# Kernel optimization log

Hardware: AMD Instinct MI355X
Metric: run time of the kernel (lower is better)

Reference implementation:

```python
import jax, jax.numpy as jnp
import numpy as np

B, N, X_DIM, Y_DIM, K = 256, 65536, 32, 64, 8
SIGMA_INIT = 0.01

def setup_inputs() -> dict:
    key = jax.random.key(0)
    k1, k2, k3, k4 = jax.random.split(key, 4)
    return {
        "x": jax.random.normal(k1, (B, X_DIM), dtype=jnp.float32),
        "pos_matrix": jax.random.normal(k2, (N, X_DIM), dtype=jnp.float32),
        "project_matrix": jax.random.normal(k3, (N, X_DIM, K), dtype=jnp.float32),
        "color_matrix": jax.random.normal(k4, (N, Y_DIM), dtype=jnp.float32),
        "sigma_matrix": jnp.full((N, K), SIGMA_INIT, dtype=jnp.float32),
    }

def reference(x, pos_matrix, project_matrix, color_matrix, sigma_matrix):
    # x_diff = (x[:,None,:] - pos[None,:,:]) @ P  -> (B, N, k)
    # computed without materializing (B, N, x_dim):
    xP = jnp.einsum('bi,nio->bno', x, project_matrix)          # (B, N, k)
    posP = jnp.einsum('ni,nio->no', pos_matrix, project_matrix)  # (N, k)
    x_diff = xP - posP[None, :, :]                               # (B, N, k)
    # Gaussian kernel per modality
    g = jnp.exp(-x_diff ** 2 / (2.0 * sigma_matrix ** 2))        # (B, N, k)
    # color = g^T @ color_matrix per batch -> (B, k, y_dim)
    color = jnp.einsum('bnk,ny->bky', g, color_matrix)
    return color
```

## Files before the change

kernel.cpp:

```cpp
#include <hip/hip_runtime.h>


typedef __attribute__((ext_vector_type(8))) short short8;
typedef __attribute__((ext_vector_type(4))) float f32x4;

#define NTOT   65536
#define XD     32
#define YD     64
#define KK     8
#define META_BYTES (NTOT*KK*8)
#define PART_FLOATS 32768
#define NCHUNKS 2048
#define CSTR   40

__device__ __forceinline__ void gload16(const void* g, void* l) {
  __builtin_amdgcn_global_load_lds(
      (const __attribute__((address_space(1))) unsigned*)g,
      (__attribute__((address_space(3))) unsigned*)l, 16, 0, 0);
}

union FragU { unsigned u[4]; short8 s8; };

__global__ __launch_bounds__(256)
void gaf_pre(const float* __restrict__ pos, const float* __restrict__ proj,
             const float* __restrict__ sig, float2* __restrict__ meta) {
  int gid = blockIdx.x * 256 + threadIdx.x;
  int n = gid >> 3, k = gid & 7;
  const float*  pk = proj + (size_t)n * XD * KK + k;
  const float4* pg = (const float4*)(pos + (size_t)n * XD);
  float d = 0.f;
#pragma unroll
  for (int j = 0; j < 8; ++j) {
    float4 v = pg[j];
    d = fmaf(v.x, pk[(4*j+0)*KK], d);
    d = fmaf(v.y, pk[(4*j+1)*KK], d);
    d = fmaf(v.z, pk[(4*j+2)*KK], d);
    d = fmaf(v.w, pk[(4*j+3)*KK], d);
  }
  float s = sig[gid];
  meta[gid] = make_float2(d, -0.72134752044448169f / (s * s));
}

__global__ __launch_bounds__(512, 4)
void gaf_main(const float* __restrict__ x, const float* __restrict__ proj,
              const float* __restrict__ colr, const float2* __restrict__ meta,
              float* __restrict__ partial, int NCH, int NR) {
  __shared__ __align__(16) unsigned short sPool[16*512*2 + 64*CSTR];
  __shared__ float sPosP[8][36];
  __shared__ float sInv[8][36];
  __shared__ __align__(16) float rawP[32*260];
  unsigned short* sPb0 = sPool;
  unsigned short* sPb1 = sPool + 16*512;
  unsigned short (*sCol)[CSTR] = (unsigned short(*)[CSTR])(sPool + 2*16*512);

  const int t = threadIdx.x, l = t & 63, w = t >> 6;

  int nr, sblk;
  {
    const int gid = blockIdx.x;
    if ((NR & 7) == 0) {
      const int xcd = gid & 7, j = gid >> 3;
      nr   = xcd * (NR >> 3) + (j >> 2);
      sblk = j & 3;
    } else { nr = gid >> 2; sblk = gid & 3; }
  }

  const int bt = w & 3, k0 = (w >> 2) * 4;
  const int lc = l & 15, lg = l >> 4;
  const int cbeg = nr * NCH;
  int cend = cbeg + NCH; if (cend > NCHUNKS) cend = NCHUNKS;

  float* pb = partial + (size_t)(nr * 4 + sblk) * PART_FLOATS;
  if (cbeg >= cend) {
    float4 z = {0.f,0.f,0.f,0.f};
#pragma unroll
    for (int r = 0; r < PART_FLOATS/4/512; ++r) ((float4*)pb)[t + r*512] = z;
    return;
  }

  short8 xf0, xf1;
  {
    const int brow = sblk*64 + bt*16 + lc;
    const float4* xr = (const float4*)(x + (size_t)brow*XD + lg*8);
    float4 u0 = xr[0], u1 = xr[1];
    float xv[8] = {u0.x,u0.y,u0.z,u0.w,u1.x,u1.y,u1.z,u1.w};
#pragma unroll
    for (int j = 0; j < 8; ++j) {
      unsigned u = __float_as_uint(xv[j]);
      unsigned short h0 = (unsigned short)(u >> 16);
      float r1 = xv[j] - __uint_as_float(u & 0xFFFF0000u);
      unsigned ur = __float_as_uint(r1);
      ur += 0x7FFFu + ((ur >> 16) & 1u);
      xf0[j] = (short)h0;
      xf1[j] = (short)(unsigned short)(ur >> 16);
    }
  }

  f32x4 acc[4][4];
#pragma unroll
  for (int a = 0; a < 4; ++a)
#pragma unroll
    for (int b = 0; b < 4; ++b) acc[a][b] = (f32x4){0.f,0.f,0.f,0.f};

  const int kp  = l & 1;
  const int ipL = (l >> 1) & 3;
  const int nS  = ((l >> 3) & 7) | ((w & 3) << 3);
  const int sS  = nS >> 4;
  const int ldst= (nS & 15);

  auto ISSUE_P = [&](int c) {
    const float4* Pg = (const float4*)(proj + (size_t)c * 32 * XD * KK);
#pragma unroll
    for (int r2 = 0; r2 < 4; ++r2) {
      const int nd = w + r2*8;
      gload16(Pg + nd*64 + l, &rawP[nd*260]);
    }
  };

  ISSUE_P(cbeg);
  for (int c = cbeg; c < cend; ++c) {
    __syncthreads();
    const int yq = w*8 + (l>>3);
    const int nq = (l&7)*4;
    const float* cb = colr + (size_t)(c*32 + nq)*YD + yq;
    float c0 = cb[0], c1 = cb[YD], c2 = cb[2*YD], c3 = cb[3*YD];
    float2 mpf;
    if (t < 256) mpf = meta[(size_t)c * 256 + t];
    {
      const float4* raw4 = (const float4*)rawP;
#pragma unroll
      for (int r = 0; r < 2; ++r) {
        const int ip = ipL | (((w >> 2) & 1) << 2) | (r << 3);
        const int f0 = nS * 65 + ip * 4 + kp;
        float4 va = raw4[f0], vb = raw4[f0 + 2];
        const int l_dst = ldst | ((ip >> 2) << 4);
        const int wd = ip & 3;
        float ea[4] = {va.x, va.y, va.z, va.w};
        float eb[4] = {vb.x, vb.y, vb.z, vb.w};
#pragma unroll
        for (int jj = 0; jj < 4; ++jj) {
          const int ks = (kp*4 + jj)*2 + sS;
          unsigned hi, lo;
          asm("v_cvt_pk_bf16_f32 %0, %1, %2" : "=v"(hi) : "v"(ea[jj]), "v"(eb[jj]));
          float r0 = ea[jj] - __uint_as_float(hi << 16);
          float r1 = eb[jj] - __uint_as_float(hi & 0xFFFF0000u);
          asm("v_cvt_pk_bf16_f32 %0, %1, %2" : "=v"(lo) : "v"(r0), "v"(r1));
          ((unsigned*)sPb0)[ks*256 + l_dst*4 + wd] = hi;
          ((unsigned*)sPb1)[ks*256 + l_dst*4 + wd] = lo;
        }
      }
    }
    {
      unsigned w0, w1;
      asm("v_cvt_pk_bf16_f32 %0, %1, %2" : "=v"(w0) : "v"(c0), "v"(c1));
      asm("v_cvt_pk_bf16_f32 %0, %1, %2" : "=v"(w1) : "v"(c2), "v"(c3));
      *(uint2*)&sCol[yq][nq] = make_uint2(w0, w1);
    }
    if (t < 256) { sPosP[t&7][t>>3] = mpf.x; sInv[t&7][t>>3] = mpf.y; }
    __syncthreads();
    if (c + 1 < cend) ISSUE_P(c + 1);

    __builtin_amdgcn_s_setprio(1);
#pragma unroll
    for (int kk = 0; kk < 4; ++kk) {
      const int k = k0 + kk;
      FragU gb;
      {
        short8 p0 = *(const short8*)&sPb0[(k*2+0)*512 + l*8];
        short8 p1 = *(const short8*)&sPb1[(k*2+0)*512 + l*8];
        f32x4 S = (f32x4){0.f,0.f,0.f,0.f};
        S = __builtin_amdgcn_mfma_f32_16x16x32_bf16(p1, xf1, S, 0, 0, 0);
        S = __builtin_amdgcn_mfma_f32_16x16x32_bf16(p1, xf0, S, 0, 0, 0);
        S = __builtin_amdgcn_mfma_f32_16x16x32_bf16(p0, xf1, S, 0, 0, 0);
        S = __builtin_amdgcn_mfma_f32_16x16x32_bf16(p0, xf0, S, 0, 0, 0);
        float4 pp = *(const float4*)&sPosP[k][lg*4];
        float4 iv = *(const float4*)&sInv[k][lg*4];
        float d0 = S[0]-pp.x, d1 = S[1]-pp.y, d2 = S[2]-pp.z, d3 = S[3]-pp.w;
        float g0 = __builtin_amdgcn_exp2f(d0*d0*iv.x);
        float g1 = __builtin_amdgcn_exp2f(d1*d1*iv.y);
        float g2 = __builtin_amdgcn_exp2f(d2*d2*iv.z);
        float g3 = __builtin_amdgcn_exp2f(d3*d3*iv.w);
        asm("v_cvt_pk_bf16_f32 %0, %1, %2" : "=v"(gb.u[0]) : "v"(g0), "v"(g1));
        asm("v_cvt_pk_bf16_f32 %0, %1, %2" : "=v"(gb.u[1]) : "v"(g2), "v"(g3));
      }
      {
        short8 p0 = *(const short8*)&sPb0[(k*2+1)*512 + l*8];
        short8 p1 = *(const short8*)&sPb1[(k*2+1)*512 + l*8];
        f32x4 S = (f32x4){0.f,0.f,0.f,0.f};
        S = __builtin_amdgcn_mfma_f32_16x16x32_bf16(p1, xf1, S, 0, 0, 0);
        S = __builtin_amdgcn_mfma_f32_16x16x32_bf16(p1, xf0, S, 0, 0, 0);
        S = __builtin_amdgcn_mfma_f32_16x16x32_bf16(p0, xf1, S, 0, 0, 0);
        S = __builtin_amdgcn_mfma_f32_16x16x32_bf16(p0, xf0, S, 0, 0, 0);
        float4 pp = *(const float4*)&sPosP[k][16 + lg*4];
        float4 iv = *(const float4*)&sInv[k][16 + lg*4];
        float d0 = S[0]-pp.x, d1 = S[1]-pp.y, d2 = S[2]-pp.z, d3 = S[3]-pp.w;
        float g0 = __builtin_amdgcn_exp2f(d0*d0*iv.x);
        float g1 = __builtin_amdgcn_exp2f(d1*d1*iv.y);
        float g2 = __builtin_amdgcn_exp2f(d2*d2*iv.z);
        float g3 = __builtin_amdgcn_exp2f(d3*d3*iv.w);
        asm("v_cvt_pk_bf16_f32 %0, %1, %2" : "=v"(gb.u[2]) : "v"(g0), "v"(g1));
        asm("v_cvt_pk_bf16_f32 %0, %1, %2" : "=v"(gb.u[3]) : "v"(g2), "v"(g3));
      }
#pragma unroll
      for (int ys = 0; ys < 4; ++ys) {
        FragU af;
        *(uint2*)&af.u[0] = *(const uint2*)&sCol[ys*16 + lc][lg*4];
        *(uint2*)&af.u[2] = *(const uint2*)&sCol[ys*16 + lc][16 + lg*4];
        acc[kk][ys] = __builtin_amdgcn_mfma_f32_16x16x32_bf16(af.s8, gb.s8,
                                                              acc[kk][ys], 0, 0, 0);
      }
    }
    __builtin_amdgcn_s_setprio(0);
  }
  __syncthreads();

  float* epi = (float*)sPool + w * (64*17);
#pragma unroll
  for (int kk = 0; kk < 4; ++kk) {
    const int k = k0 + kk;
#pragma unroll
    for (int ys = 0; ys < 4; ++ys) {
#pragma unroll
      for (int r = 0; r < 4; ++r)
        epi[(ys*16 + lg*4 + r)*17 + lc] = acc[kk][ys][r];
    }
    __syncthreads();
#pragma unroll
    for (int it = 0; it < 4; ++it) {
      int bi = it*4 + lg, y0 = lc*4;
      float4 v = { epi[(y0+0)*17 + bi], epi[(y0+1)*17 + bi],
                   epi[(y0+2)*17 + bi], epi[(y0+3)*17 + bi] };
      *(float4*)&pb[(size_t)(bt*16 + bi)*512 + k*64 + y0] = v;
    }
    __syncthreads();
  }
}

__global__ __launch_bounds__(512)
void gaf_reduce(const float* __restrict__ partial, float* __restrict__ out, int NR) {
  const int b = blockIdx.x;
  const int s = b >> 6, bl = b & 63;
  const int t = threadIdx.x;
  float a0 = 0.f, a1 = 0.f, a2 = 0.f, a3 = 0.f;
  int nr = 0;
  for (; nr + 4 <= NR; nr += 4) {
    a0 += partial[(size_t)((nr+0)*4 + s)*PART_FLOATS + bl*512 + t];
    a1 += partial[(size_t)((nr+1)*4 + s)*PART_FLOATS + bl*512 + t];
    a2 += partial[(size_t)((nr+2)*4 + s)*PART_FLOATS + bl*512 + t];
    a3 += partial[(size_t)((nr+3)*4 + s)*PART_FLOATS + bl*512 + t];
  }
  for (; nr < NR; ++nr)
    a0 += partial[(size_t)(nr*4 + s)*PART_FLOATS + bl*512 + t];
  out[(size_t)b*512 + t] = (a0 + a1) + (a2 + a3);
}

extern "C" void kernel_launch(void* const* d_in, const int* in_sizes, int n_in,
                              void* d_out, int out_size, void* d_ws, size_t ws_size,
                              hipStream_t stream) {
  const float* x    = (const float*)d_in[0];
  const float* pos  = (const float*)d_in[1];
  const float* proj = (const float*)d_in[2];
  const float* colr = (const float*)d_in[3];
  const float* sig  = (const float*)d_in[4];
  float* out = (float*)d_out;

  float2* meta    = (float2*)d_ws;
  float*  partial = (float*)((char*)d_ws + META_BYTES);

  size_t avail = (ws_size > META_BYTES) ? ws_size - META_BYTES : 0;
  int NR = (int)(avail / (4ull * PART_FLOATS * 4ull));
  if (NR > 128) NR = 128;
  if (NR < 1)  NR = 1;
  if (NR >= 8) NR &= ~7;
  int NCH = (NCHUNKS + NR - 1) / NR;

  gaf_pre<<<(NTOT*KK)/256, 256, 0, stream>>>(pos, proj, sig, meta);
  gaf_main<<<4*NR, 512, 0, stream>>>(x, proj, colr, meta, partial, NCH, NR);
  gaf_reduce<<<256, 512, 0, stream>>>(partial, out, NR);
}
```

Baseline: 100.0 us.

## Fuse posP and inverse-sigma precompute into main kernel, drop pre-pass

Removes the separate gaf_pre kernel that computed pos·P projections and inverse sigma terms into a workspace buffer. The main kernel now loads each chunk's pos rows asynchronously into LDS next to the projection tile it already stages, and computes the dot products and inverse sigma in-loop. This saves one kernel launch and a second full read of the projection matrix, at the cost of extra LDS, extra per-chunk ALU work and an LDS-bank-conflicted dot product on the critical path between barriers.

Result: no change. 99.67 us, median of 2 (-0.4%).

```diff
diff --git a/kernel.cpp b/kernel.cpp
--- a/kernel.cpp
+++ b/kernel.cpp
@@ -8,7 +8,6 @@
 #define XD     32
 #define YD     64
 #define KK     8
-#define META_BYTES (NTOT*KK*8)
 #define PART_FLOATS 32768
 #define NCHUNKS 2048
 #define CSTR   40
@@ -21,34 +20,16 @@
 
 union FragU { unsigned u[4]; short8 s8; };
 
-__global__ __launch_bounds__(256)
-void gaf_pre(const float* __restrict__ pos, const float* __restrict__ proj,
-             const float* __restrict__ sig, float2* __restrict__ meta) {
-  int gid = blockIdx.x * 256 + threadIdx.x;
-  int n = gid >> 3, k = gid & 7;
-  const float*  pk = proj + (size_t)n * XD * KK + k;
-  const float4* pg = (const float4*)(pos + (size_t)n * XD);
-  float d = 0.f;
-#pragma unroll
-  for (int j = 0; j < 8; ++j) {
-    float4 v = pg[j];
-    d = fmaf(v.x, pk[(4*j+0)*KK], d);
-    d = fmaf(v.y, pk[(4*j+1)*KK], d);
-    d = fmaf(v.z, pk[(4*j+2)*KK], d);
-    d = fmaf(v.w, pk[(4*j+3)*KK], d);
-  }
-  float s = sig[gid];
-  meta[gid] = make_float2(d, -0.72134752044448169f / (s * s));
-}
-
 __global__ __launch_bounds__(512, 4)
-void gaf_main(const float* __restrict__ x, const float* __restrict__ proj,
-              const float* __restrict__ colr, const float2* __restrict__ meta,
+void gaf_main(const float* __restrict__ x, const float* __restrict__ pos,
+              const float* __restrict__ proj, const float* __restrict__ colr,
+              const float* __restrict__ sig,
               float* __restrict__ partial, int NCH, int NR) {
   __shared__ __align__(16) unsigned short sPool[16*512*2 + 64*CSTR];
   __shared__ float sPosP[8][36];
   __shared__ float sInv[8][36];
   __shared__ __align__(16) float rawP[32*260];
+  __shared__ __align__(16) float rawPos[32*32];
   unsigned short* sPb0 = sPool;
   unsigned short* sPb1 = sPool + 16*512;
   unsigned short (*sCol)[CSTR] = (unsigned short(*)[CSTR])(sPool + 2*16*512);
@@ -115,6 +96,11 @@
       const int nd = w + r2*8;
       gload16(Pg + nd*64 + l, &rawP[nd*260]);
     }
+    if (t < 256) {
+      const float4* Sg = (const float4*)pos;
+      gload16(Sg + ((size_t)(c*32 + (t & 31)) * 8 + (t >> 5)),
+              &rawPos[(t >> 6) * 256]);
+    }
   };
 
   ISSUE_P(cbeg);
@@ -124,8 +110,8 @@
     const int nq = (l&7)*4;
     const float* cb = colr + (size_t)(c*32 + nq)*YD + yq;
     float c0 = cb[0], c1 = cb[YD], c2 = cb[2*YD], c3 = cb[3*YD];
-    float2 mpf;
-    if (t < 256) mpf = meta[(size_t)c * 256 + t];
+    float sgv = 0.f;
+    if (t < 256) sgv = sig[(size_t)c * 256 + t];
     {
       const float4* raw4 = (const float4*)rawP;
 #pragma unroll
@@ -156,7 +142,23 @@
       asm("v_cvt_pk_bf16_f32 %0, %1, %2" : "=v"(w1) : "v"(c2), "v"(c3));
       *(uint2*)&sCol[yq][nq] = make_uint2(w0, w1);
     }
-    if (t < 256) { sPosP[t&7][t>>3] = mpf.x; sInv[t&7][t>>3] = mpf.y; }
+    if (t < 256) {
+      const int n = t >> 3, k = t & 7;
+      float d = 0.f;
+#pragma unroll
+      for (int j = 0; j < 8; ++j) {
+        float p0 = rawPos[j*128 + n*4 + 0];
+        float p1 = rawPos[j*128 + n*4 + 1];
+        float p2 = rawPos[j*128 + n*4 + 2];
+        float p3 = rawPos[j*128 + n*4 + 3];
+        d = fmaf(p0, rawP[n*260 + (4*j+0)*8 + k], d);
+        d = fmaf(p1, rawP[n*260 + (4*j+1)*8 + k], d);
+        d = fmaf(p2, rawP[n*260 + (4*j+2)*8 + k], d);
+        d = fmaf(p3, rawP[n*260 + (4*j+3)*8 + k], d);
+      }
+      sPosP[k][n] = d;
+      sInv[k][n]  = -0.72134752044448169f / (sgv * sgv);
+    }
     __syncthreads();
     if (c + 1 < cend) ISSUE_P(c + 1);
 
@@ -264,17 +266,14 @@
   const float* sig  = (const float*)d_in[4];
   float* out = (float*)d_out;
 
-  float2* meta    = (float2*)d_ws;
-  float*  partial = (float*)((char*)d_ws + META_BYTES);
-
-  size_t avail = (ws_size > META_BYTES) ? ws_size - META_BYTES : 0;
-  int NR = (int)(avail / (4ull * PART_FLOATS * 4ull));
+  float* partial = (float*)d_ws;
+
+  int NR = (int)(ws_size / (4ull * PART_FLOATS * 4ull));
   if (NR > 128) NR = 128;
   if (NR < 1)  NR = 1;
   if (NR >= 8) NR &= ~7;
   int NCH = (NCHUNKS + NR - 1) / NR;
 
-  gaf_pre<<<(NTOT*KK)/256, 256, 0, stream>>>(pos, proj, sig, meta);
-  gaf_main<<<4*NR, 512, 0, stream>>>(x, proj, colr, meta, partial, NCH, NR);
+  gaf_main<<<4*NR, 512, 0, stream>>>(x, pos, proj, colr, sig, partial, NCH, NR);
   gaf_reduce<<<256, 512, 0, stream>>>(partial, out, NR);
 }
```
